# Kernel optimization log

Measured on AMD Instinct MI355X. Metric: run time of the kernel, lower is better.

Reference implementation:

```python
import jax, jax.numpy as jnp
import numpy as np

B, C, Ci, H, W = 8, 256, 128, 64, 64
EPS = 1e-5


def conv1x1(x, w, b):
    # x: [B,C,H,W], w: [O,C], b: [O] -> [B,O,H,W]
    return jnp.einsum('bchw,oc->bohw', x, w) + b[None, :, None, None]


def maxpool2(x):
    b, c, h, w = x.shape
    return x.reshape(b, c, h // 2, 2, w // 2, 2).max(axis=(3, 5))


def setup_inputs() -> dict:
    key = jax.random.key(0)
    ks = jax.random.split(key, 12)
    s_in = 1.0 / np.sqrt(C)
    s_ic = 1.0 / np.sqrt(Ci)
    return {
        'x': jax.random.normal(ks[0], (B, C, H, W), dtype=jnp.float32),
        'g_w': jax.random.normal(ks[1], (Ci, C), dtype=jnp.float32) * s_in,
        'g_b': jax.random.normal(ks[2], (Ci,), dtype=jnp.float32) * 0.01,
        'theta_w': jax.random.normal(ks[3], (Ci, C), dtype=jnp.float32) * s_in,
        'theta_b': jax.random.normal(ks[4], (Ci,), dtype=jnp.float32) * 0.01,
        'phi_w': jax.random.normal(ks[5], (Ci, C), dtype=jnp.float32) * s_in,
        'phi_b': jax.random.normal(ks[6], (Ci,), dtype=jnp.float32) * 0.01,
        'W_w': jax.random.normal(ks[7], (C, Ci), dtype=jnp.float32) * s_ic,
        'W_b': jax.random.normal(ks[8], (C,), dtype=jnp.float32) * 0.01,
        'bn_gamma': jax.random.normal(ks[9], (C,), dtype=jnp.float32) * 0.1 + 1.0,
        'bn_beta': jax.random.normal(ks[10], (C,), dtype=jnp.float32) * 0.1,
        'bn_mean': jnp.zeros((C,), dtype=jnp.float32),
        'bn_var': jax.random.uniform(ks[11], (C,), dtype=jnp.float32) * 0.5 + 0.75,
    }


def reference(x, g_w, g_b, theta_w, theta_b, phi_w, phi_b, W_w, W_b, bn_gamma, bn_beta, bn_mean, bn_var):
    b = x.shape[0]
    # g and phi: 1x1 conv then 2x2 max-pool (sub_sample=True)
    g_x = maxpool2(conv1x1(x, g_w, g_b)).reshape(b, Ci, -1)          # [B,Ci,Np]
    g_x = jnp.transpose(g_x, (0, 2, 1))                               # [B,Np,Ci]
    theta_x = conv1x1(x, theta_w, theta_b).reshape(b, Ci, -1)         # [B,Ci,N]
    theta_x = jnp.transpose(theta_x, (0, 2, 1))                       # [B,N,Ci]
    phi_x = maxpool2(conv1x1(x, phi_w, phi_b)).reshape(b, Ci, -1)     # [B,Ci,Np]
    f = jnp.einsum('bnc,bcm->bnm', theta_x, phi_x)                    # [B,N,Np]
    f_div_C = jax.nn.softmax(f, axis=-1)                              # embedded_gaussian: plain softmax, no scaling
    y = jnp.einsum('bnm,bmc->bnc', f_div_C, g_x)                      # [B,N,Ci]
    y = jnp.transpose(y, (0, 2, 1)).reshape(b, Ci, H, W)              # [B,Ci,H,W]
    # W: 1x1 conv + BatchNorm (inference form with running stats)
    W_y = conv1x1(y, W_w, W_b)
    inv = bn_gamma / jnp.sqrt(bn_var + EPS)
    W_y = (W_y - bn_mean[None, :, None, None]) * inv[None, :, None, None] + bn_beta[None, :, None, None]
    return W_y + x
```

## Files before the change

### kernel.cpp

```cpp
#include <hip/hip_runtime.h>
#include <math.h>

#define Bn   8
#define Cc   256
#define Cin  128
#define Hh   64
#define Ww   64
#define Nn   4096
#define Npl  1024
#define EPSf 1e-5f

typedef __attribute__((ext_vector_type(8))) short    short8;
typedef __attribute__((ext_vector_type(8))) _Float16 half8;
typedef __attribute__((ext_vector_type(4))) float    floatx4;

__device__ __forceinline__ unsigned short f2bf(float f) {
    unsigned int u = __float_as_uint(f);
    u += 0x7fffu + ((u >> 16) & 1u);
    return (unsigned short)(u >> 16);
}
__device__ __forceinline__ unsigned short f2h(float f) {
    _Float16 h = (_Float16)f;
    return __builtin_bit_cast(unsigned short, h);
}
__device__ __forceinline__ float h2f(unsigned short u) {
    return (float)__builtin_bit_cast(_Float16, u);
}

__device__ __forceinline__ unsigned int cvtpk_bf16(float lo, float hi) {
    unsigned int r;
    asm("v_cvt_pk_bf16_f32 %0, %1, %2" : "=v"(r) : "v"(lo), "v"(hi));
    return r;
}

__device__ __forceinline__ void gload_lds16(const unsigned short* g, unsigned short* l) {
    __builtin_amdgcn_global_load_lds(
        (const __attribute__((address_space(1))) unsigned int*)g,
        (__attribute__((address_space(3))) unsigned int*)l, 16, 0, 0);
}

__global__ __launch_bounds__(256) void k_prep(
    const float* __restrict__ g_w, const float* __restrict__ th_w,
    const float* __restrict__ ph_w,
    const float* __restrict__ W_w, const float* __restrict__ W_b,
    const float* __restrict__ gamma, const float* __restrict__ beta,
    const float* __restrict__ mean,  const float* __restrict__ var,
    unsigned short* __restrict__ gWh,
    unsigned short* __restrict__ thWh, unsigned short* __restrict__ thWl,
    unsigned short* __restrict__ phWh, unsigned short* __restrict__ phWl,
    unsigned short* __restrict__ Wh, float* __restrict__ cvec)
{
    int i = blockIdx.x * 256 + threadIdx.x;
    if (i < 98304) {
        int seg = i >> 15;
        int idx = i & 32767;
        int o = idx >> 8;
        int c = idx & 255;
        int p = (((o >> 4) * 8 + (c >> 5)) * 64
                 + ((c >> 3) & 3) * 16 + (o & 15)) * 8 + (c & 7);
        float v = (seg == 0 ? g_w : (seg == 1 ? th_w : ph_w))[idx];
        unsigned short hi = f2h(v);
        if (seg == 0) gWh[p] = hi;
        else {
            (seg == 1 ? thWh : phWh)[p] = hi;
            (seg == 1 ? thWl : phWl)[p] = f2h(v - h2f(hi));
        }
    } else {
        int j = i - 98304;
        int o = j >> 7;
        float inv = gamma[o] * rsqrtf(var[o] + EPSf);
        Wh[j] = f2h(W_w[j] * inv);
        if (j < Cc) {
            float invi = gamma[j] * rsqrtf(var[j] + EPSf);
            cvec[j] = (W_b[j] - mean[j]) * invi + beta[j];
        }
    }
}

#define XPAD 264

__global__ __launch_bounds__(512, 4) void k_conv3(
    const float* __restrict__ x,
    const unsigned short* __restrict__ gWh,
    const unsigned short* __restrict__ thWh, const unsigned short* __restrict__ thWl,
    const unsigned short* __restrict__ phWh, const unsigned short* __restrict__ phWl,
    const float* __restrict__ g_b, const float* __restrict__ th_b,
    const float* __restrict__ ph_b,
    unsigned short* __restrict__ thetaT,
    unsigned short* __restrict__ gPc,
    unsigned short* __restrict__ phiPt)
{
    __shared__ __align__(16) unsigned short Xhi[64 * XPAD];
    __shared__ __align__(16) unsigned short Xlo[64 * XPAD];

    const int t    = threadIdx.x;
    const int w    = t >> 6;
    const int l    = t & 63;
    const int quad = l >> 4;
    const int l16  = l & 15;
    const int b    = blockIdx.x >> 6;
    const int tile = blockIdx.x & 63;
    const int ty   = tile >> 1;
    const int tx   = tile & 1;

    {
        const float4* xg = (const float4*)x;
        unsigned int* XhiW = (unsigned int*)Xhi;
        unsigned int* XloW = (unsigned int*)Xlo;
        #pragma unroll
        for (int it = 0; it < 4; ++it) {
            int idx = t + 512 * it;
            int c2  = idx >> 4;
            int p4  = idx & 15;
            int n   = (2 * ty + (p4 >> 3)) * Ww + tx * 32 + (p4 & 7) * 4;
            float4 va = xg[((size_t)(b * Cc + 2 * c2) * Nn + n) >> 2];
            float4 vb = xg[((size_t)(b * Cc + 2 * c2 + 1) * Nn + n) >> 2];
            const float fa[4] = {va.x, va.y, va.z, va.w};
            const float fb[4] = {vb.x, vb.y, vb.z, vb.w};
            #pragma unroll
            for (int i = 0; i < 4; ++i) {
                int px = p4 * 4 + i;
                unsigned short ha = f2h(fa[i]), hb = f2h(fb[i]);
                unsigned short la = f2h(fa[i] - h2f(ha));
                unsigned short lb = f2h(fb[i] - h2f(hb));
                XhiW[px * 132 + c2] = (unsigned int)ha | ((unsigned int)hb << 16);
                XloW[px * 132 + c2] = (unsigned int)la | ((unsigned int)lb << 16);
            }
        }
    }
    __syncthreads();

    floatx4 acc[3][4] = {};

    #pragma unroll 2
    for (int kd = 0; kd < 8; ++kd) {
        half8 bhi[4], blo[4];
        #pragma unroll
        for (int nt = 0; nt < 4; ++nt) {
            bhi[nt] = *(const half8*)&Xhi[(nt * 16 + l16) * XPAD + kd * 32 + quad * 8];
            blo[nt] = *(const half8*)&Xlo[(nt * 16 + l16) * XPAD + kd * 32 + quad * 8];
        }
        #pragma unroll
        for (int ti = 0; ti < 3; ++ti) {
            int seg = ti;
            size_t aoff = (size_t)((w * 8 + kd) * 512 + l * 8);
            const unsigned short* wh = (seg == 0 ? gWh : (seg == 1 ? thWh : phWh));
            half8 ah = *(const half8*)&wh[aoff];
            #pragma unroll
            for (int nt = 0; nt < 4; ++nt)
                acc[ti][nt] = __builtin_amdgcn_mfma_f32_16x16x32_f16(ah, bhi[nt], acc[ti][nt], 0, 0, 0);
            if (seg != 0) {
                const unsigned short* wl = (seg == 1 ? thWl : phWl);
                half8 al = *(const half8*)&wl[aoff];
                #pragma unroll
                for (int nt = 0; nt < 4; ++nt) {
                    acc[ti][nt] = __builtin_amdgcn_mfma_f32_16x16x32_f16(ah, blo[nt], acc[ti][nt], 0, 0, 0);
                    acc[ti][nt] = __builtin_amdgcn_mfma_f32_16x16x32_f16(al, bhi[nt], acc[ti][nt], 0, 0, 0);
                }
            }
        }
    }

    #pragma unroll
    for (int ti = 0; ti < 3; ++ti) {
        int seg = ti;
        int ol  = w * 16 + quad * 4;
        if (seg == 1) {
            float b0 = th_b[ol], b1 = th_b[ol + 1], b2 = th_b[ol + 2], b3 = th_b[ol + 3];
            #pragma unroll
            for (int nt = 0; nt < 4; ++nt) {
                int n = (2 * ty + (nt >> 1)) * Ww + tx * 32 + (nt & 1) * 16 + l16;
                ushort4 v;
                v.x = f2h(acc[ti][nt][0] + b0);
                v.y = f2h(acc[ti][nt][1] + b1);
                v.z = f2h(acc[ti][nt][2] + b2);
                v.w = f2h(acc[ti][nt][3] + b3);
                *(ushort4*)&thetaT[((size_t)b * Nn + n) * Cin + ol] = v;
            }
        } else {
            const float* bb = (seg == 0 ? g_b : ph_b);
            float b0 = bb[ol], b1 = bb[ol + 1], b2 = bb[ol + 2], b3 = bb[ol + 3];
            #pragma unroll
            for (int pp = 0; pp < 2; ++pp) {
                float pm[4];
                #pragma unroll
                for (int r = 0; r < 4; ++r) {
                    float m = fmaxf(acc[ti][pp][r], acc[ti][pp + 2][r]);
                    pm[r] = fmaxf(m, __shfl_xor(m, 1, 64));
                }
                int np = ty * 32 + tx * 16 + pp * 8 + (l16 >> 1);
                if ((l16 & 1) == 0) {
                    if (seg == 0) {
                        gPc[((size_t)b * Cin + ol + 0) * Npl + np] = f2bf(pm[0] + b0);
                        gPc[((size_t)b * Cin + ol + 1) * Npl + np] = f2bf(pm[1] + b1);
                        gPc[((size_t)b * Cin + ol + 2) * Npl + np] = f2bf(pm[2] + b2);
                        gPc[((size_t)b * Cin + ol + 3) * Npl + np] = f2bf(pm[3] + b3);
                    } else {
                        ushort4 v;
                        v.x = f2h(pm[0] + b0); v.y = f2h(pm[1] + b1);
                        v.z = f2h(pm[2] + b2); v.w = f2h(pm[3] + b3);
                        *(ushort4*)&phiPt[((size_t)b * Npl + np) * Cin + ol] = v;
                    }
                }
            }
        }
    }
}

__device__ __forceinline__ void stage_kv(
    unsigned short* smem, int sel, int chg, int b, int grp, int wq,
    int mK, int gK, int cV, int gV,
    const unsigned short* __restrict__ phiPt,
    const unsigned short* __restrict__ gPc)
{
    unsigned short* Kb = smem + sel * 16384;
    if (grp == 0) {
        #pragma unroll
        for (int j = 0; j < 4; ++j) {
            int slot = wq * 4 + j;
            int m  = slot * 4 + mK;
            int gs = gK ^ (m & 7);
            gload_lds16(&phiPt[((size_t)b * Npl + chg * 64 + m) * Cin + gs * 8],
                        &Kb[slot * 512]);
        }
    } else {
        unsigned short* Vb = Kb + 8192;
        #pragma unroll
        for (int j = 0; j < 4; ++j) {
            int slot = wq * 4 + j;
            int c  = slot * 8 + cV;
            int gs = gV ^ (c & 7);
            gload_lds16(&gPc[((size_t)b * Cin + c) * Npl + chg * 64 + gs * 8],
                        &Vb[slot * 512]);
        }
    }
}

#define SSHIFT 20.0f

__global__ __launch_bounds__(512, 2) void k_attn_out(
    const unsigned short* __restrict__ thetaT,
    const unsigned short* __restrict__ phiPt,
    const unsigned short* __restrict__ gPc,
    const unsigned short* __restrict__ Wh,
    const float* __restrict__ cvec,
    const float* __restrict__ x,
    float* __restrict__ out)
{
    __shared__ __align__(16) unsigned short smem[65536];

    const int t    = threadIdx.x;
    const int w    = t >> 6;
    const int wq   = w & 3;
    const int grp  = w >> 2;
    const int l    = t & 63;
    const int quad = l >> 4;
    const int l16  = l & 15;
    const int bid  = blockIdx.x;
    const int wid  = (bid & 7) * 32 + (bid >> 3);
    const int b    = wid >> 5;
    const int qb   = wid & 31;
    const int n0   = qb * 128;

    uint4 qr0[4], qr1[4];
    #pragma unroll
    for (int kd = 0; kd < 4; ++kd) {
        qr0[kd] = *(const uint4*)&thetaT[((size_t)b * Nn + n0 + wq * 32 + l16) * Cin
                                         + kd * 32 + quad * 8];
        qr1[kd] = *(const uint4*)&thetaT[((size_t)b * Nn + n0 + wq * 32 + 16 + l16) * Cin
                                         + kd * 32 + quad * 8];
    }
    #pragma unroll
    for (int kd = 0; kd < 4; ++kd) {
        asm volatile("" : "+v"(qr0[kd].x), "+v"(qr0[kd].y), "+v"(qr0[kd].z), "+v"(qr0[kd].w));
        asm volatile("" : "+v"(qr1[kd].x), "+v"(qr1[kd].y), "+v"(qr1[kd].z), "+v"(qr1[kd].w));
    }
    half8 qf0[4], qf1[4];
    #pragma unroll
    for (int kd = 0; kd < 4; ++kd) {
        qf0[kd] = __builtin_bit_cast(half8, qr0[kd]);
        qf1[kd] = __builtin_bit_cast(half8, qr1[kd]);
    }

    floatx4 yacc0[8] = {}, yacc1[8] = {};
    float liq0 = 0.f, liq1 = 0.f;

    const int mK = l >> 4;
    const int gK = l & 15;
    const int cV = l >> 3;
    const int gV = l & 7;

    #pragma unroll
    for (int pc = 0; pc < 3; ++pc)
        stage_kv(smem, pc, pc, b, grp, wq, mK, gK, cV, gV, phiPt, gPc);
    asm volatile("s_waitcnt vmcnt(8)" ::: "memory");
    __builtin_amdgcn_s_barrier();

    for (int ch = 0; ch < 16; ++ch) {
        if (ch < 13)
            stage_kv(smem, (ch + 3) & 3, ch + 3, b, grp, wq, mK, gK, cV, gV, phiPt, gPc);

        const unsigned short* Ks = smem + (ch & 3) * 16384;
        const unsigned short* Vt = Ks + 8192;

        floatx4 sacc0[2] = {}, sacc1[2] = {};
        #pragma unroll
        for (int mtl = 0; mtl < 2; ++mtl) {
            int mt = grp * 2 + mtl;
            #pragma unroll
            for (int kd = 0; kd < 4; ++kd) {
                half8 kf = *(const half8*)&Ks[(mt * 16 + l16) * 128
                                              + (((kd * 4 + quad) ^ (l16 & 7)) << 3)];
                sacc0[mtl] = __builtin_amdgcn_mfma_f32_16x16x32_f16(kf, qf0[kd], sacc0[mtl], 0, 0, 0);
                sacc1[mtl] = __builtin_amdgcn_mfma_f32_16x16x32_f16(kf, qf1[kd], sacc1[mtl], 0, 0, 0);
            }
        }

        short8 pf0, pf1;
        {
            float e0[4], e1[4];
            #pragma unroll
            for (int r = 0; r < 4; ++r) {
                e0[r] = __expf(sacc0[0][r] - SSHIFT);
                e1[r] = __expf(sacc0[1][r] - SSHIFT);
                liq0 += e0[r] + e1[r];
            }
            unsigned int a0 = cvtpk_bf16(e0[0], e0[1]);
            unsigned int a1 = cvtpk_bf16(e1[0], e1[1]);
            unsigned int b0 = cvtpk_bf16(e0[2], e0[3]);
            unsigned int b1 = cvtpk_bf16(e1[2], e1[3]);
            asm volatile("v_permlane32_swap_b32 %0, %1" : "+v"(a0), "+v"(a1));
            asm volatile("v_permlane16_swap_b32 %0, %1" : "+v"(a0), "+v"(a1));
            asm volatile("v_permlane32_swap_b32 %0, %1" : "+v"(b0), "+v"(b1));
            asm volatile("v_permlane16_swap_b32 %0, %1" : "+v"(b0), "+v"(b1));
            uint4 pw; pw.x = a0; pw.y = b0; pw.z = a1; pw.w = b1;
            pf0 = __builtin_bit_cast(short8, pw);
        }
        {
            float e0[4], e1[4];
            #pragma unroll
            for (int r = 0; r < 4; ++r) {
                e0[r] = __expf(sacc1[0][r] - SSHIFT);
                e1[r] = __expf(sacc1[1][r] - SSHIFT);
                liq1 += e0[r] + e1[r];
            }
            unsigned int a0 = cvtpk_bf16(e0[0], e0[1]);
            unsigned int a1 = cvtpk_bf16(e1[0], e1[1]);
            unsigned int b0 = cvtpk_bf16(e0[2], e0[3]);
            unsigned int b1 = cvtpk_bf16(e1[2], e1[3]);
            asm volatile("v_permlane32_swap_b32 %0, %1" : "+v"(a0), "+v"(a1));
            asm volatile("v_permlane16_swap_b32 %0, %1" : "+v"(a0), "+v"(a1));
            asm volatile("v_permlane32_swap_b32 %0, %1" : "+v"(b0), "+v"(b1));
            asm volatile("v_permlane16_swap_b32 %0, %1" : "+v"(b0), "+v"(b1));
            uint4 pw; pw.x = a0; pw.y = b0; pw.z = a1; pw.w = b1;
            pf1 = __builtin_bit_cast(short8, pw);
        }

        #pragma unroll
        for (int ct = 0; ct < 8; ++ct) {
            short8 vf = *(const short8*)&Vt[(ct * 16 + l16) * 64
                                            + (((grp * 4 + quad) ^ (l16 & 7)) << 3)];
            yacc0[ct] = __builtin_amdgcn_mfma_f32_16x16x32_bf16(pf0, vf, yacc0[ct], 0, 0, 0);
            yacc1[ct] = __builtin_amdgcn_mfma_f32_16x16x32_bf16(pf1, vf, yacc1[ct], 0, 0, 0);
        }

        if (ch < 13)       asm volatile("s_waitcnt vmcnt(8)" ::: "memory");
        else if (ch == 13) asm volatile("s_waitcnt vmcnt(4)" ::: "memory");
        else if (ch == 14) asm volatile("s_waitcnt vmcnt(0)" ::: "memory");
        __builtin_amdgcn_s_barrier();
    }

    liq0 += __shfl_xor(liq0, 16, 64);
    liq0 += __shfl_xor(liq0, 32, 64);
    liq1 += __shfl_xor(liq1, 16, 64);
    liq1 += __shfl_xor(liq1, 32, 64);

    float* cbuf = (float*)smem;
    const int ci0 = ((wq * 2 + 0) * 64 + l) * 33;
    const int ci1 = ((wq * 2 + 1) * 64 + l) * 33;
    if (grp == 1) {
        #pragma unroll
        for (int ct = 0; ct < 8; ++ct)
            #pragma unroll
            for (int r = 0; r < 4; ++r) {
                cbuf[ci0 + ct * 4 + r] = yacc0[ct][r];
                cbuf[ci1 + ct * 4 + r] = yacc1[ct][r];
            }
        cbuf[ci0 + 32] = liq0;
        cbuf[ci1 + 32] = liq1;
    }
    __syncthreads();
    if (grp == 0) {
        #pragma unroll
        for (int ct = 0; ct < 8; ++ct)
            #pragma unroll
            for (int r = 0; r < 4; ++r) {
                yacc0[ct][r] += cbuf[ci0 + ct * 4 + r];
                yacc1[ct][r] += cbuf[ci1 + ct * 4 + r];
            }
        liq0 += cbuf[ci0 + 32];
        liq1 += cbuf[ci1 + 32];
    }
    __syncthreads();

    {
        unsigned short* Ws = smem + 16384;
        #pragma unroll
        for (int j = 0; j < 8; ++j) {
            int slot = w * 8 + j;
            int row  = slot * 4 + mK;
            int gs   = gK ^ (row & 7);
            gload_lds16(&Wh[(size_t)row * Cin + gs * 8], &Ws[slot * 512]);
        }
    }

    if (grp == 0) {
        unsigned int* Yw = (unsigned int*)smem;
        #pragma unroll
        for (int r = 0; r < 4; ++r) {
            float lr0 = __shfl(liq0, quad * 4 + r, 64);
            float lr1 = __shfl(liq1, quad * 4 + r, 64);
            float il0 = 1.0f / lr0;
            float il1 = 1.0f / lr1;
            int q0 = wq * 32 + quad * 4 + r;
            int q1 = q0 + 16;
            #pragma unroll
            for (int ct = 0; ct < 8; ++ct) {
                unsigned int h0 = f2h(yacc0[ct][r] * il0);
                unsigned int p0 = (unsigned int)__shfl_xor((int)h0, 1, 64);
                unsigned int h1 = f2h(yacc1[ct][r] * il1);
                unsigned int p1 = (unsigned int)__shfl_xor((int)h1, 1, 64);
                if ((l16 & 1) == 0) {
                    int g = ct * 2 + (l16 >> 3);
                    Yw[q0 * 64 + (((g ^ (q0 & 7)) << 2) | ((l16 & 7) >> 1))] = h0 | (p0 << 16);
                    Yw[q1 * 64 + (((g ^ (q1 & 7)) << 2) | ((l16 & 7) >> 1))] = h1 | (p1 << 16);
                }
            }
        }
    }
    asm volatile("s_waitcnt vmcnt(0)" ::: "memory");
    __syncthreads();

    const unsigned short* Ys = smem;
    const unsigned short* Ws = smem + 16384;

    half8 af[2][4];
    #pragma unroll
    for (int mt = 0; mt < 2; ++mt)
        #pragma unroll
        for (int kd = 0; kd < 4; ++kd) {
            int row = w * 32 + mt * 16 + l16;
            af[mt][kd] = *(const half8*)&Ws[row * 128
                                            + (((kd * 4 + quad) ^ (l16 & 7)) << 3)];
        }

    floatx4 acc[2][8] = {};
    #pragma unroll
    for (int nt = 0; nt < 8; ++nt) {
        half8 bfr[4];
        #pragma unroll
        for (int kd = 0; kd < 4; ++kd)
            bfr[kd] = *(const half8*)&Ys[(nt * 16 + l16) * 128
                                         + (((kd * 4 + quad) ^ (l16 & 7)) << 3)];
        #pragma unroll
        for (int mt = 0; mt < 2; ++mt)
            #pragma unroll
            for (int kd = 0; kd < 4; ++kd)
                acc[mt][nt] = __builtin_amdgcn_mfma_f32_16x16x32_f16(af[mt][kd], bfr[kd], acc[mt][nt], 0, 0, 0);
    }

    #pragma unroll
    for (int mt = 0; mt < 2; ++mt) {
        #pragma unroll
        for (int r = 0; r < 4; ++r) {
            int o = w * 32 + mt * 16 + quad * 4 + r;
            float cv = cvec[o];
            #pragma unroll
            for (int nt = 0; nt < 8; ++nt) {
                size_t gi = ((size_t)(b * Cc + o)) * Nn + n0 + nt * 16 + l16;
                out[gi] = acc[mt][nt][r] + cv + x[gi];
            }
        }
    }
}

extern "C" void kernel_launch(void* const* d_in, const int* in_sizes, int n_in,
                              void* d_out, int out_size, void* d_ws, size_t ws_size,
                              hipStream_t stream) {
    const float* x    = (const float*)d_in[0];
    const float* g_w  = (const float*)d_in[1];
    const float* g_b  = (const float*)d_in[2];
    const float* th_w = (const float*)d_in[3];
    const float* th_b = (const float*)d_in[4];
    const float* ph_w = (const float*)d_in[5];
    const float* ph_b = (const float*)d_in[6];
    const float* W_w  = (const float*)d_in[7];
    const float* W_b  = (const float*)d_in[8];
    const float* gmm  = (const float*)d_in[9];
    const float* bta  = (const float*)d_in[10];
    const float* mmn  = (const float*)d_in[11];
    const float* vvr  = (const float*)d_in[12];
    float* out = (float*)d_out;

    unsigned short* thetaT = (unsigned short*)d_ws;
    unsigned short* phiPt  = thetaT + (size_t)4194304;
    unsigned short* gPc    = phiPt + (size_t)1048576;
    unsigned short* Wh     = gPc + (size_t)1048576;
    unsigned short* gWh    = Wh + 32768;
    unsigned short* thWh   = gWh + 32768;
    unsigned short* thWl   = thWh + 32768;
    unsigned short* phWh   = thWl + 32768;
    unsigned short* phWl   = phWh + 32768;
    float*          cvec   = (float*)(phWl + 32768);

    k_prep<<<dim3(512), dim3(256), 0, stream>>>(
        g_w, th_w, ph_w, W_w, W_b, gmm, bta, mmn, vvr,
        gWh, thWh, thWl, phWh, phWl, Wh, cvec);
    k_conv3<<<dim3(Bn * 64), dim3(512), 0, stream>>>(
        x, gWh, thWh, thWl, phWh, phWl, g_b, th_b, ph_b, thetaT, gPc, phiPt);
    k_attn_out<<<dim3(Bn * 32), dim3(512), 0, stream>>>(
        thetaT, phiPt, gPc, Wh, cvec, x, out);
}
```

Baseline: 156.9 us.

## Software-pipeline QK^T scores one chunk ahead of PV accumulation in attention loop

Restructures the attention main loop so the QK^T MFMAs for chunk ch+1 are issued before the PV MFMAs for chunk ch, and the exp/bf16 packing of the next scores happens after the PV step. A prologue computes the first chunk's probabilities, and the vmcnt waits and barriers are shifted so the next K buffer must be resident one iteration earlier. The aim is to overlap the exp/permlane work with MFMA latency and break the dependency chain between score computation and value accumulation. The cost is higher register pressure from extra live score accumulators, tighter load-wait timing on the prefetch ring, and an added barrier before the epilogue.

```diff
diff --git a/kernel.cpp b/kernel.cpp
--- a/kernel.cpp
+++ b/kernel.cpp
@@ -236,6 +236,26 @@
     }
 }
 
+__device__ __forceinline__ short8 pack_pf(floatx4 s0, floatx4 s1, float& liq) {
+    float e0[4], e1[4];
+    #pragma unroll
+    for (int r = 0; r < 4; ++r) {
+        e0[r] = __expf(s0[r] - 20.0f);
+        e1[r] = __expf(s1[r] - 20.0f);
+        liq += e0[r] + e1[r];
+    }
+    unsigned int a0 = cvtpk_bf16(e0[0], e0[1]);
+    unsigned int a1 = cvtpk_bf16(e1[0], e1[1]);
+    unsigned int b0 = cvtpk_bf16(e0[2], e0[3]);
+    unsigned int b1 = cvtpk_bf16(e1[2], e1[3]);
+    asm volatile("v_permlane32_swap_b32 %0, %1" : "+v"(a0), "+v"(a1));
+    asm volatile("v_permlane16_swap_b32 %0, %1" : "+v"(a0), "+v"(a1));
+    asm volatile("v_permlane32_swap_b32 %0, %1" : "+v"(b0), "+v"(b1));
+    asm volatile("v_permlane16_swap_b32 %0, %1" : "+v"(b0), "+v"(b1));
+    uint4 pw; pw.x = a0; pw.y = b0; pw.z = a1; pw.w = b1;
+    return __builtin_bit_cast(short8, pw);
+}
+
 #define SSHIFT 20.0f
 
 __global__ __launch_bounds__(512, 2) void k_attn_out(
@@ -296,78 +316,66 @@
     asm volatile("s_waitcnt vmcnt(8)" ::: "memory");
     __builtin_amdgcn_s_barrier();
 
+    short8 pfA0, pfA1;
+    {
+        const unsigned short* Ks = smem;
+        floatx4 s00[2] = {}, s10[2] = {};
+        #pragma unroll
+        for (int mtl = 0; mtl < 2; ++mtl) {
+            int mt = grp * 2 + mtl;
+            #pragma unroll
+            for (int kd = 0; kd < 4; ++kd) {
+                half8 kf = *(const half8*)&Ks[(mt * 16 + l16) * 128
+                                              + (((kd * 4 + quad) ^ (l16 & 7)) << 3)];
+                s00[mtl] = __builtin_amdgcn_mfma_f32_16x16x32_f16(kf, qf0[kd], s00[mtl], 0, 0, 0);
+                s10[mtl] = __builtin_amdgcn_mfma_f32_16x16x32_f16(kf, qf1[kd], s10[mtl], 0, 0, 0);
+            }
+        }
+        pfA0 = pack_pf(s00[0], s00[1], liq0);
+        pfA1 = pack_pf(s10[0], s10[1], liq1);
+    }
+    asm volatile("s_waitcnt vmcnt(4)" ::: "memory");
+    __builtin_amdgcn_s_barrier();
+
     for (int ch = 0; ch < 16; ++ch) {
         if (ch < 13)
             stage_kv(smem, (ch + 3) & 3, ch + 3, b, grp, wq, mK, gK, cV, gV, phiPt, gPc);
 
-        const unsigned short* Ks = smem + (ch & 3) * 16384;
-        const unsigned short* Vt = Ks + 8192;
-
-        floatx4 sacc0[2] = {}, sacc1[2] = {};
-        #pragma unroll
-        for (int mtl = 0; mtl < 2; ++mtl) {
-            int mt = grp * 2 + mtl;
-            #pragma unroll
-            for (int kd = 0; kd < 4; ++kd) {
-                half8 kf = *(const half8*)&Ks[(mt * 16 + l16) * 128
-                                              + (((kd * 4 + quad) ^ (l16 & 7)) << 3)];
-                sacc0[mtl] = __builtin_amdgcn_mfma_f32_16x16x32_f16(kf, qf0[kd], sacc0[mtl], 0, 0, 0);
-                sacc1[mtl] = __builtin_amdgcn_mfma_f32_16x16x32_f16(kf, qf1[kd], sacc1[mtl], 0, 0, 0);
-            }
-        }
-
-        short8 pf0, pf1;
+        floatx4 s0n[2] = {}, s1n[2] = {};
+        if (ch < 15) {
+            const unsigned short* Ksn = smem + ((ch + 1) & 3) * 16384;
+            #pragma unroll
+            for (int mtl = 0; mtl < 2; ++mtl) {
+                int mt = grp * 2 + mtl;
+                #pragma unroll
+                for (int kd = 0; kd < 4; ++kd) {
+                    half8 kf = *(const half8*)&Ksn[(mt * 16 + l16) * 128
+                                                   + (((kd * 4 + quad) ^ (l16 & 7)) << 3)];
+                    s0n[mtl] = __builtin_amdgcn_mfma_f32_16x16x32_f16(kf, qf0[kd], s0n[mtl], 0, 0, 0);
+                    s1n[mtl] = __builtin_amdgcn_mfma_f32_16x16x32_f16(kf, qf1[kd], s1n[mtl], 0, 0, 0);
+                }
+            }
+        }
+
         {
-            float e0[4], e1[4];
-            #pragma unroll
-            for (int r = 0; r < 4; ++r) {
-                e0[r] = __expf(sacc0[0][r] - SSHIFT);
-                e1[r] = __expf(sacc0[1][r] - SSHIFT);
-                liq0 += e0[r] + e1[r];
-            }
-            unsigned int a0 = cvtpk_bf16(e0[0], e0[1]);
-            unsigned int a1 = cvtpk_bf16(e1[0], e1[1]);
-            unsigned int b0 = cvtpk_bf16(e0[2], e0[3]);
-            unsigned int b1 = cvtpk_bf16(e1[2], e1[3]);
-            asm volatile("v_permlane32_swap_b32 %0, %1" : "+v"(a0), "+v"(a1));
-            asm volatile("v_permlane16_swap_b32 %0, %1" : "+v"(a0), "+v"(a1));
-            asm volatile("v_permlane32_swap_b32 %0, %1" : "+v"(b0), "+v"(b1));
-            asm volatile("v_permlane16_swap_b32 %0, %1" : "+v"(b0), "+v"(b1));
-            uint4 pw; pw.x = a0; pw.y = b0; pw.z = a1; pw.w = b1;
-            pf0 = __builtin_bit_cast(short8, pw);
-        }
-        {
-            float e0[4], e1[4];
-            #pragma unroll
-            for (int r = 0; r < 4; ++r) {
-                e0[r] = __expf(sacc1[0][r] - SSHIFT);
-                e1[r] = __expf(sacc1[1][r] - SSHIFT);
-                liq1 += e0[r] + e1[r];
-            }
-            unsigned int a0 = cvtpk_bf16(e0[0], e0[1]);
-            unsigned int a1 = cvtpk_bf16(e1[0], e1[1]);
-            unsigned int b0 = cvtpk_bf16(e0[2], e0[3]);
-            unsigned int b1 = cvtpk_bf16(e1[2], e1[3]);
-            asm volatile("v_permlane32_swap_b32 %0, %1" : "+v"(a0), "+v"(a1));
-            asm volatile("v_permlane16_swap_b32 %0, %1" : "+v"(a0), "+v"(a1));
-            asm volatile("v_permlane32_swap_b32 %0, %1" : "+v"(b0), "+v"(b1));
-            asm volatile("v_permlane16_swap_b32 %0, %1" : "+v"(b0), "+v"(b1));
-            uint4 pw; pw.x = a0; pw.y = b0; pw.z = a1; pw.w = b1;
-            pf1 = __builtin_bit_cast(short8, pw);
-        }
-
-        #pragma unroll
-        for (int ct = 0; ct < 8; ++ct) {
-            short8 vf = *(const short8*)&Vt[(ct * 16 + l16) * 64
-                                            + (((grp * 4 + quad) ^ (l16 & 7)) << 3)];
-            yacc0[ct] = __builtin_amdgcn_mfma_f32_16x16x32_bf16(pf0, vf, yacc0[ct], 0, 0, 0);
-            yacc1[ct] = __builtin_amdgcn_mfma_f32_16x16x32_bf16(pf1, vf, yacc1[ct], 0, 0, 0);
-        }
-
-        if (ch < 13)       asm volatile("s_waitcnt vmcnt(8)" ::: "memory");
-        else if (ch == 13) asm volatile("s_waitcnt vmcnt(4)" ::: "memory");
-        else if (ch == 14) asm volatile("s_waitcnt vmcnt(0)" ::: "memory");
-        __builtin_amdgcn_s_barrier();
+            const unsigned short* Vt = smem + (ch & 3) * 16384 + 8192;
+            #pragma unroll
+            for (int ct = 0; ct < 8; ++ct) {
+                short8 vf = *(const short8*)&Vt[(ct * 16 + l16) * 64
+                                                + (((grp * 4 + quad) ^ (l16 & 7)) << 3)];
+                yacc0[ct] = __builtin_amdgcn_mfma_f32_16x16x32_bf16(pfA0, vf, yacc0[ct], 0, 0, 0);
+                yacc1[ct] = __builtin_amdgcn_mfma_f32_16x16x32_bf16(pfA1, vf, yacc1[ct], 0, 0, 0);
+            }
+        }
+
+        if (ch < 15) {
+            pfA0 = pack_pf(s0n[0], s0n[1], liq0);
+            pfA1 = pack_pf(s1n[0], s1n[1], liq1);
+        }
+
+        if (ch <= 12)      asm volatile("s_waitcnt vmcnt(4)" ::: "memory");
+        else if (ch == 13) asm volatile("s_waitcnt vmcnt(0)" ::: "memory");
+        if (ch <= 13) __builtin_amdgcn_s_barrier();
     }
 
     liq0 += __shfl_xor(liq0, 16, 64);
@@ -375,6 +383,7 @@
     liq1 += __shfl_xor(liq1, 16, 64);
     liq1 += __shfl_xor(liq1, 32, 64);
 
+    __syncthreads();
     float* cbuf = (float*)smem;
     const int ci0 = ((wq * 2 + 0) * 64 + l) * 33;
     const int ci1 = ((wq * 2 + 1) * 64 + l) * 33;
```

Result: no change. 154.4 us (-1.6%).
